# Kernel tuning notes

Hardware: AMD Instinct MI355X
Metric: run time of the kernel (lower is better)

## Reference

```python
import jax, jax.numpy as jnp
import numpy as np

H = 2048
I = 8192
E = 8
EI = I // E  # expert_intermediate_size = 1024


def setup_inputs() -> dict:
    key = jax.random.key(0)
    k1, k2, k3 = jax.random.split(key, 3)
    B, N = 4, 4096
    x = jax.random.normal(k1, (B, N, H), dtype=jnp.float32)
    position_ids = jnp.arange(B * N, dtype=jnp.int64).reshape(B, N)
    gate_up_proj = 0.02 * jax.random.normal(k2, (E, H, EI * 2), dtype=jnp.float32)
    down_proj = 0.02 * jax.random.normal(k3, (E, EI, H), dtype=jnp.float32)
    return {"x": x, "position_ids": position_ids,
            "gate_up_proj": gate_up_proj, "down_proj": down_proj}


def reference(x, position_ids, gate_up_proj, down_proj):
    # x: [B,N,H]; position_ids: [B,N] (or [N]); expert = pos % E.
    B, N, Hdim = x.shape
    if position_ids.ndim == 1:
        position_ids = jnp.broadcast_to(position_ids[None, :], (B, N))
    eids = (position_ids % E).reshape(B * N)
    flat = x.reshape(B * N, Hdim)

    # Modulo routing is perfectly balanced (N % E == 0 with sequential ids),
    # so group tokens by expert (stable sort) and run dense per-expert GEMMs
    # instead of per-token gathered-weight bmm (same math, no weight blowup).
    T = B * N
    order = jnp.argsort(eids)          # stable in jax -> tokens grouped by expert
    xg = flat[order].reshape(E, T // E, Hdim)            # [E, T/E, H]
    gu = jnp.einsum('ebh,ehk->ebk', xg, gate_up_proj)    # [E, T/E, 2*EI]
    gate, up = gu[..., :EI], gu[..., EI:]
    inter = jax.nn.silu(gate) * up                       # [E, T/E, EI]
    outg = jnp.einsum('ebi,eih->ebh', inter, down_proj)  # [E, T/E, H]
    out = jnp.zeros((T, Hdim), dtype=x.dtype).at[order].set(outg.reshape(T, Hdim))
    return out.reshape(B, N, Hdim)
```

## Files before the change

kernel.cpp:

```cpp
#include <hip/hip_runtime.h>
#include <hip/hip_bf16.h>

typedef unsigned short u16;
typedef __attribute__((ext_vector_type(8))) short short8;
typedef __attribute__((ext_vector_type(8))) unsigned short u16x8;
typedef __attribute__((ext_vector_type(4))) float f32x4;

#define H_DIM 2048
#define EI_DIM 1024
#define NEXP 8

template <int V> struct IC { static constexpr int value = V; };

__device__ __forceinline__ u16 f2bf(float f) {
  __hip_bfloat16 h = __float2bfloat16(f);
  return __builtin_bit_cast(unsigned short, h);
}

__device__ __forceinline__ void load_lds16(const void* g, void* lds) {
  __builtin_amdgcn_global_load_lds(
      (const __attribute__((address_space(1))) unsigned int*)g,
      (__attribute__((address_space(3))) unsigned int*)lds, 16, 0, 0);
}

__global__ void hist_kernel(const int* __restrict__ pid, int* __restrict__ hist) {
  int seg = blockIdx.x, lane = threadIdx.x;
  int eid = pid[seg * 64 + lane] & 7;
#pragma unroll
  for (int e = 0; e < NEXP; ++e) {
    unsigned long long m = __ballot(eid == e);
    if (lane == 0) hist[e * 256 + seg] = __popcll(m);
  }
}

__global__ void scan_kernel(const int* __restrict__ hist, int* __restrict__ base,
                            int* __restrict__ offcnt, int T) {
  __shared__ int lds[256];
  int tid = threadIdx.x;
  int v[8], s = 0;
#pragma unroll
  for (int j = 0; j < 8; ++j) { v[j] = hist[tid * 8 + j]; s += v[j]; }
  lds[tid] = s;
  __syncthreads();
  for (int d = 1; d < 256; d <<= 1) {
    int t = (tid >= d) ? lds[tid - d] : 0;
    __syncthreads();
    lds[tid] += t;
    __syncthreads();
  }
  int run = lds[tid] - s;
#pragma unroll
  for (int j = 0; j < 8; ++j) { base[tid * 8 + j] = run; run += v[j]; }
  __syncthreads();
  if (tid < NEXP) {
    int o = base[tid * 256];
    int nx = (tid < NEXP - 1) ? base[(tid + 1) * 256] : T;
    offcnt[tid] = o;
    offcnt[8 + tid] = nx - o;
  }
}

__global__ void rank_kernel(const int* __restrict__ pid, const int* __restrict__ base,
                            int* __restrict__ order) {
  int seg = blockIdx.x, lane = threadIdx.x;
  int t = seg * 64 + lane;
  int eid = pid[t] & 7;
  unsigned long long below = (1ull << lane) - 1ull;
#pragma unroll
  for (int e = 0; e < NEXP; ++e) {
    unsigned long long m = __ballot(eid == e);
    if (eid == e) {
      int r = __popcll(m & below);
      order[base[e * 256 + seg] + r] = t;
    }
  }
}

__global__ __launch_bounds__(256) void transpose_bf16(const float* __restrict__ in,
                                                      u16* __restrict__ out, int R, int C) {
  __shared__ u16 tile[64][65];
  int nbr = R >> 6, nbc = C >> 6;
  int per_e = nbr * nbc;
  int bx = blockIdx.x;
  int e = bx / per_e, rem = bx % per_e;
  int tr = rem % nbr, tc = rem / nbr;
  const float* ine = in + (size_t)e * R * C;
  u16* oute = out + (size_t)e * R * C;
  int r0 = tr * 64, c0 = tc * 64;
  int tid = threadIdx.x;
  int lrow = tid >> 4, lc4 = (tid & 15) * 4;
#pragma unroll
  for (int p = 0; p < 4; ++p) {
    int rl = p * 16 + lrow;
    float4 v = *(const float4*)&ine[(size_t)(r0 + rl) * C + c0 + lc4];
    tile[rl][lc4 + 0] = f2bf(v.x);
    tile[rl][lc4 + 1] = f2bf(v.y);
    tile[rl][lc4 + 2] = f2bf(v.z);
    tile[rl][lc4 + 3] = f2bf(v.w);
  }
  __syncthreads();
#pragma unroll
  for (int q = 0; q < 16; ++q) {
    int idx = q * 256 + tid;
    int jr = idx >> 6, hc = idx & 63;
    oute[(size_t)(c0 + jr) * R + r0 + hc] = tile[hc][jr];
  }
}

__global__ __launch_bounds__(256) void gather_x(const float* __restrict__ x,
                                                const int* __restrict__ order,
                                                u16* __restrict__ xg) {
  int g = blockIdx.x;
  int t = order[g];
  const float* src = x + (size_t)t * H_DIM;
  u16* dst = xg + (size_t)g * H_DIM;
  int c = threadIdx.x * 8;
  float4 a = *(const float4*)&src[c];
  float4 b = *(const float4*)&src[c + 4];
  u16x8 v;
  v[0] = f2bf(a.x); v[1] = f2bf(a.y); v[2] = f2bf(a.z); v[3] = f2bf(a.w);
  v[4] = f2bf(b.x); v[5] = f2bf(b.y); v[6] = f2bf(b.z); v[7] = f2bf(b.w);
  *(u16x8*)&dst[c] = v;
}

template <int KTOT, int KIND>
__global__ __launch_bounds__(512, 2) void gemm8_kernel(
    const u16* __restrict__ A, const u16* __restrict__ Bmat, void* __restrict__ outp,
    const int* __restrict__ offcnt, const int* __restrict__ order, int T, int MT) {
  constexpr int NK = KTOT / 64;
  constexpr int ASTR = (KIND == 0) ? H_DIM : EI_DIM;
  constexpr int BSTR = ASTR;
  constexpr size_t BEXP = (size_t)2048 * BSTR;
  __shared__ u16 As[2][2][8192];
  __shared__ u16 Bs[2][2][8192];

  int nwg = gridDim.x;
  int bid = blockIdx.x;
  int bx = ((nwg & 7) == 0) ? ((bid & 7) * (nwg >> 3) + (bid >> 3)) : bid;

  int nt = bx & 7;
  int rest = bx >> 3;
  int mt = rest % MT;
  int e = rest / MT;
  int off = offcnt[e], cnt = offcnt[8 + e];
  if (mt * 256 >= cnt) return;

  const u16* Be = Bmat + (size_t)e * BEXP;
  int tid = threadIdx.x, w = tid >> 6, l = tid & 63;
  int wm = w >> 2, wn = w & 3, lr = l & 15, lg = l >> 4;

  const u16* aSrc[2];
  const u16* bSrc[2];
#pragma unroll
  for (int j = 0; j < 2; ++j) {
    int r = j * 128 + (tid >> 2);
    int c = tid & 3;
    int sw = (r >> 1) & 3;
    int grow = min(off + mt * 256 + r, T - 1);
    aSrc[j] = A + (size_t)grow * ASTR + ((c ^ sw) * 8);
    int n;
    if (KIND == 0) {
      int q = r >> 4, rr = r & 15;
      n = ((q & 2) ? EI_DIM : 0) + nt * 128 + ((q >> 2) << 5) + ((q & 1) << 4) + rr;
    } else {
      n = nt * 256 + r;
    }
    bSrc[j] = Be + (size_t)n * BSTR + ((c ^ sw) * 8);
  }

  auto stageA = [&](int kt, int kh, int buf) {
#pragma unroll
    for (int j = 0; j < 2; ++j)
      load_lds16(aSrc[j] + kt * 64 + kh * 32, &As[buf][kh][j * 4096 + w * 512]);
  };
  auto stageB = [&](int kt, int kh, int buf) {
#pragma unroll
    for (int j = 0; j < 2; ++j)
      load_lds16(bSrc[j] + kt * 64 + kh * 32, &Bs[buf][kh][j * 4096 + w * 512]);
  };

  int cidx = (lg ^ ((lr >> 1) & 3)) * 8;
  int aRow0 = wm * 128 + lr;
  int bRow0 = wn * 64 + lr;

  short8 av[4], bv[4];
  auto loadA4 = [&](int buf, int kh, int h) {
#pragma unroll
    for (int mm = 0; mm < 4; ++mm)
      av[mm] = *(const short8*)&As[buf][kh][(aRow0 + (h * 4 + mm) * 16) * 32 + cidx];
  };
  auto loadB4 = [&](int buf, int kh) {
#pragma unroll
    for (int nn = 0; nn < 4; ++nn)
      bv[nn] = *(const short8*)&Bs[buf][kh][(bRow0 + nn * 16) * 32 + cidx];
  };

  f32x4 acc[8][4];
#pragma unroll
  for (int m = 0; m < 8; ++m)
#pragma unroll
    for (int nn = 0; nn < 4; ++nn) acc[m][nn] = {0.f, 0.f, 0.f, 0.f};

  auto MFMA_H = [&](auto HC) {
    constexpr int h = decltype(HC)::value;
    __builtin_amdgcn_s_setprio(1);
#pragma unroll
    for (int mm = 0; mm < 4; ++mm)
#pragma unroll
      for (int nn = 0; nn < 4; ++nn)
        acc[h * 4 + mm][nn] =
            __builtin_amdgcn_mfma_f32_16x16x32_bf16(av[mm], bv[nn], acc[h * 4 + mm][nn], 0, 0, 0);
    __builtin_amdgcn_s_setprio(0);
  };

  stageA(0, 0, 0); stageB(0, 0, 0); stageA(0, 1, 0); stageB(0, 1, 0);
  stageB(1, 0, 1); stageA(1, 0, 1); stageB(1, 1, 1);
  asm volatile("s_waitcnt vmcnt(6)" ::: "memory");
  __builtin_amdgcn_s_barrier();
  __builtin_amdgcn_sched_barrier(0);

  auto TILE = [&](int t, auto BC) {
    constexpr int b = decltype(BC)::value;
    constexpr int bn = b ^ 1;
    loadA4(b, 0, 0);
    loadB4(b, 0);
    stageA(t + 1, 1, bn);
    __builtin_amdgcn_s_barrier();
    MFMA_H(IC<0>{});
    __builtin_amdgcn_s_barrier();
    __builtin_amdgcn_sched_barrier(0);
    loadA4(b, 0, 1);
    stageB(t + 2, 0, b);
    __builtin_amdgcn_s_barrier();
    MFMA_H(IC<1>{});
    __builtin_amdgcn_s_barrier();
    __builtin_amdgcn_sched_barrier(0);
    loadA4(b, 1, 0);
    loadB4(b, 1);
    stageA(t + 2, 0, b);
    __builtin_amdgcn_s_barrier();
    MFMA_H(IC<0>{});
    __builtin_amdgcn_s_barrier();
    __builtin_amdgcn_sched_barrier(0);
    loadA4(b, 1, 1);
    stageB(t + 2, 1, b);
    __builtin_amdgcn_s_barrier();
    MFMA_H(IC<1>{});
    asm volatile("s_waitcnt vmcnt(6)" ::: "memory");
    __builtin_amdgcn_s_barrier();
    __builtin_amdgcn_sched_barrier(0);
  };

#pragma unroll 1
  for (int t = 0; t < NK - 3; t += 2) {
    TILE(t, IC<0>{});
    TILE(t + 1, IC<1>{});
  }

  {
    loadA4(0, 0, 0);
    loadB4(0, 0);
    stageA(NK - 1, 1, 1);
    MFMA_H(IC<0>{});
    loadA4(0, 0, 1);
    MFMA_H(IC<1>{});
    loadA4(0, 1, 0);
    loadB4(0, 1);
    MFMA_H(IC<0>{});
    loadA4(0, 1, 1);
    MFMA_H(IC<1>{});
    asm volatile("s_waitcnt vmcnt(0)" ::: "memory");
    __builtin_amdgcn_s_barrier();
    __builtin_amdgcn_sched_barrier(0);
    loadA4(1, 0, 0);
    loadB4(1, 0);
    MFMA_H(IC<0>{});
    loadA4(1, 0, 1);
    MFMA_H(IC<1>{});
    loadA4(1, 1, 0);
    loadB4(1, 1);
    MFMA_H(IC<0>{});
    loadA4(1, 1, 1);
    MFMA_H(IC<1>{});
  }

  if (KIND == 0) {
    u16* inter = (u16*)outp;
#pragma unroll
    for (int m = 0; m < 8; ++m)
#pragma unroll
      for (int nn = 0; nn < 2; ++nn) {
        f32x4 g = acc[m][nn], u = acc[m][nn + 2];
        int icol = nt * 128 + wn * 32 + nn * 16 + lr;
#pragma unroll
        for (int j = 0; j < 4; ++j) {
          int r = wm * 128 + m * 16 + lg * 4 + j;
          int grow = mt * 256 + r;
          if (grow < cnt) {
            float gv = g[j];
            float val = (gv / (1.f + __expf(-gv))) * u[j];
            inter[(size_t)(off + grow) * EI_DIM + icol] = f2bf(val);
          }
        }
      }
  } else {
    float* out = (float*)outp;
#pragma unroll
    for (int m = 0; m < 8; ++m)
#pragma unroll
      for (int nn = 0; nn < 4; ++nn) {
        int ncol = nt * 256 + wn * 64 + nn * 16 + lr;
#pragma unroll
        for (int j = 0; j < 4; ++j) {
          int r = wm * 128 + m * 16 + lg * 4 + j;
          int grow = mt * 256 + r;
          if (grow < cnt) {
            int tt = order[off + grow];
            out[(size_t)tt * H_DIM + ncol] = acc[m][nn][j];
          }
        }
      }
  }
}

extern "C" void kernel_launch(void* const* d_in, const int* in_sizes, int n_in,
                              void* d_out, int out_size, void* d_ws, size_t ws_size,
                              hipStream_t stream) {
  const float* x = (const float*)d_in[0];
  const int* pid = (const int*)d_in[1];
  const float* gup = (const float*)d_in[2];
  const float* dwn = (const float*)d_in[3];
  float* out = (float*)d_out;

  const int T = in_sizes[1];
  const int MT = (T + 255) / 256;

  char* ws = (char*)d_ws;
  size_t o = 0;
  auto take = [&](size_t b) { size_t r = o; o += (b + 255) & ~(size_t)255; return r; };
  int* offcnt = (int*)(ws + take(16 * 4));
  int* hist = (int*)(ws + take(2048 * 4));
  int* base = (int*)(ws + take(2052 * 4));
  int* order = (int*)(ws + take((size_t)T * 4));
  u16* xg = (u16*)(ws + take((size_t)T * H_DIM * 2));
  u16* wguT = (u16*)(ws + take((size_t)NEXP * 2048 * 2048 * 2));
  u16* wdT = (u16*)(ws + take((size_t)NEXP * 2048 * 1024 * 2));
  u16* inter = (u16*)(ws + take((size_t)T * EI_DIM * 2));

  hist_kernel<<<T / 64, 64, 0, stream>>>(pid, hist);
  scan_kernel<<<1, 256, 0, stream>>>(hist, base, offcnt, T);
  rank_kernel<<<T / 64, 64, 0, stream>>>(pid, base, order);
  transpose_bf16<<<NEXP * 32 * 32, 256, 0, stream>>>(gup, wguT, 2048, 2048);
  transpose_bf16<<<NEXP * 16 * 32, 256, 0, stream>>>(dwn, wdT, 1024, 2048);
  gather_x<<<T, 256, 0, stream>>>(x, order, xg);

  gemm8_kernel<2048, 0><<<NEXP * MT * 8, 512, 0, stream>>>(xg, wguT, inter, offcnt, order, T, MT);
  gemm8_kernel<1024, 1><<<NEXP * MT * 8, 512, 0, stream>>>(inter, wdT, out, offcnt, order, T, MT);
}
```

Measured before the change: 353.1 us.

## Make expert GEMMs persistent over fixed grid and stage down-proj output through LDS

```diff
diff --git a/kernel.cpp b/kernel.cpp
--- a/kernel.cpp
+++ b/kernel.cpp
@@ -126,7 +126,7 @@
 template <int KTOT, int KIND>
 __global__ __launch_bounds__(512, 2) void gemm8_kernel(
     const u16* __restrict__ A, const u16* __restrict__ Bmat, void* __restrict__ outp,
-    const int* __restrict__ offcnt, const int* __restrict__ order, int T, int MT) {
+    const int* __restrict__ offcnt, const int* __restrict__ order, int T) {
   constexpr int NK = KTOT / 64;
   constexpr int ASTR = (KIND == 0) ? H_DIM : EI_DIM;
   constexpr int BSTR = ASTR;
@@ -136,190 +136,205 @@
 
   int nwg = gridDim.x;
   int bid = blockIdx.x;
-  int bx = ((nwg & 7) == 0) ? ((bid & 7) * (nwg >> 3) + (bid >> 3)) : bid;
-
-  int nt = bx & 7;
-  int rest = bx >> 3;
-  int mt = rest % MT;
-  int e = rest / MT;
+  int bx = (bid & 7) * (nwg >> 3) + (bid >> 3);
+  int e = bx >> 6;
+  int s = bx & 63;
   int off = offcnt[e], cnt = offcnt[8 + e];
-  if (mt * 256 >= cnt) return;
-
   const u16* Be = Bmat + (size_t)e * BEXP;
+
   int tid = threadIdx.x, w = tid >> 6, l = tid & 63;
   int wm = w >> 2, wn = w & 3, lr = l & 15, lg = l >> 4;
-
-  const u16* aSrc[2];
-  const u16* bSrc[2];
-#pragma unroll
-  for (int j = 0; j < 2; ++j) {
-    int r = j * 128 + (tid >> 2);
-    int c = tid & 3;
-    int sw = (r >> 1) & 3;
-    int grow = min(off + mt * 256 + r, T - 1);
-    aSrc[j] = A + (size_t)grow * ASTR + ((c ^ sw) * 8);
-    int n;
-    if (KIND == 0) {
-      int q = r >> 4, rr = r & 15;
-      n = ((q & 2) ? EI_DIM : 0) + nt * 128 + ((q >> 2) << 5) + ((q & 1) << 4) + rr;
-    } else {
-      n = nt * 256 + r;
-    }
-    bSrc[j] = Be + (size_t)n * BSTR + ((c ^ sw) * 8);
-  }
-
-  auto stageA = [&](int kt, int kh, int buf) {
-#pragma unroll
-    for (int j = 0; j < 2; ++j)
-      load_lds16(aSrc[j] + kt * 64 + kh * 32, &As[buf][kh][j * 4096 + w * 512]);
-  };
-  auto stageB = [&](int kt, int kh, int buf) {
-#pragma unroll
-    for (int j = 0; j < 2; ++j)
-      load_lds16(bSrc[j] + kt * 64 + kh * 32, &Bs[buf][kh][j * 4096 + w * 512]);
-  };
-
   int cidx = (lg ^ ((lr >> 1) & 3)) * 8;
   int aRow0 = wm * 128 + lr;
   int bRow0 = wn * 64 + lr;
-
-  short8 av[4], bv[4];
-  auto loadA4 = [&](int buf, int kh, int h) {
-#pragma unroll
-    for (int mm = 0; mm < 4; ++mm)
-      av[mm] = *(const short8*)&As[buf][kh][(aRow0 + (h * 4 + mm) * 16) * 32 + cidx];
-  };
-  auto loadB4 = [&](int buf, int kh) {
-#pragma unroll
-    for (int nn = 0; nn < 4; ++nn)
-      bv[nn] = *(const short8*)&Bs[buf][kh][(bRow0 + nn * 16) * 32 + cidx];
-  };
-
-  f32x4 acc[8][4];
-#pragma unroll
-  for (int m = 0; m < 8; ++m)
-#pragma unroll
-    for (int nn = 0; nn < 4; ++nn) acc[m][nn] = {0.f, 0.f, 0.f, 0.f};
-
-  auto MFMA_H = [&](auto HC) {
-    constexpr int h = decltype(HC)::value;
-    __builtin_amdgcn_s_setprio(1);
-#pragma unroll
-    for (int mm = 0; mm < 4; ++mm)
+  int sr[2], sc[2];
+#pragma unroll
+  for (int j = 0; j < 2; ++j) {
+    sr[j] = j * 128 + (tid >> 2);
+    int c = tid & 3;
+    sc[j] = (c ^ ((sr[j] >> 1) & 3)) * 8;
+  }
+
+#pragma unroll 1
+  for (int it = s; it < 512; it += 64) {
+    int mt = it >> 3, nt = it & 7;
+    if (mt * 256 >= cnt) continue;
+
+    const u16* aSrc[2];
+    const u16* bSrc[2];
+#pragma unroll
+    for (int j = 0; j < 2; ++j) {
+      int r = sr[j];
+      int grow = min(off + mt * 256 + r, T - 1);
+      aSrc[j] = A + (size_t)grow * ASTR + sc[j];
+      int n;
+      if (KIND == 0) {
+        int q = r >> 4, rr = r & 15;
+        n = ((q & 2) ? EI_DIM : 0) + nt * 128 + ((q >> 2) << 5) + ((q & 1) << 4) + rr;
+      } else {
+        n = nt * 256 + r;
+      }
+      bSrc[j] = Be + (size_t)n * BSTR + sc[j];
+    }
+
+    auto stageA = [&](int kt, int kh, int buf) {
+#pragma unroll
+      for (int j = 0; j < 2; ++j)
+        load_lds16(aSrc[j] + kt * 64 + kh * 32, &As[buf][kh][j * 4096 + w * 512]);
+    };
+    auto stageB = [&](int kt, int kh, int buf) {
+#pragma unroll
+      for (int j = 0; j < 2; ++j)
+        load_lds16(bSrc[j] + kt * 64 + kh * 32, &Bs[buf][kh][j * 4096 + w * 512]);
+    };
+
+    short8 av[4], bv[4];
+    auto loadA4 = [&](int buf, int kh, int h) {
+#pragma unroll
+      for (int mm = 0; mm < 4; ++mm)
+        av[mm] = *(const short8*)&As[buf][kh][(aRow0 + (h * 4 + mm) * 16) * 32 + cidx];
+    };
+    auto loadB4 = [&](int buf, int kh) {
 #pragma unroll
       for (int nn = 0; nn < 4; ++nn)
-        acc[h * 4 + mm][nn] =
-            __builtin_amdgcn_mfma_f32_16x16x32_bf16(av[mm], bv[nn], acc[h * 4 + mm][nn], 0, 0, 0);
-    __builtin_amdgcn_s_setprio(0);
-  };
-
-  stageA(0, 0, 0); stageB(0, 0, 0); stageA(0, 1, 0); stageB(0, 1, 0);
-  stageB(1, 0, 1); stageA(1, 0, 1); stageB(1, 1, 1);
-  asm volatile("s_waitcnt vmcnt(6)" ::: "memory");
-  __builtin_amdgcn_s_barrier();
-  __builtin_amdgcn_sched_barrier(0);
-
-  auto TILE = [&](int t, auto BC) {
-    constexpr int b = decltype(BC)::value;
-    constexpr int bn = b ^ 1;
-    loadA4(b, 0, 0);
-    loadB4(b, 0);
-    stageA(t + 1, 1, bn);
-    __builtin_amdgcn_s_barrier();
-    MFMA_H(IC<0>{});
-    __builtin_amdgcn_s_barrier();
-    __builtin_amdgcn_sched_barrier(0);
-    loadA4(b, 0, 1);
-    stageB(t + 2, 0, b);
-    __builtin_amdgcn_s_barrier();
-    MFMA_H(IC<1>{});
-    __builtin_amdgcn_s_barrier();
-    __builtin_amdgcn_sched_barrier(0);
-    loadA4(b, 1, 0);
-    loadB4(b, 1);
-    stageA(t + 2, 0, b);
-    __builtin_amdgcn_s_barrier();
-    MFMA_H(IC<0>{});
-    __builtin_amdgcn_s_barrier();
-    __builtin_amdgcn_sched_barrier(0);
-    loadA4(b, 1, 1);
-    stageB(t + 2, 1, b);
-    __builtin_amdgcn_s_barrier();
-    MFMA_H(IC<1>{});
+        bv[nn] = *(const short8*)&Bs[buf][kh][(bRow0 + nn * 16) * 32 + cidx];
+    };
+
+    f32x4 acc[8][4];
+#pragma unroll
+    for (int m = 0; m < 8; ++m)
+#pragma unroll
+      for (int nn = 0; nn < 4; ++nn) acc[m][nn] = {0.f, 0.f, 0.f, 0.f};
+
+    auto MFMA_H = [&](auto HC) {
+      constexpr int h = decltype(HC)::value;
+      __builtin_amdgcn_s_setprio(1);
+#pragma unroll
+      for (int mm = 0; mm < 4; ++mm)
+#pragma unroll
+        for (int nn = 0; nn < 4; ++nn)
+          acc[h * 4 + mm][nn] =
+              __builtin_amdgcn_mfma_f32_16x16x32_bf16(av[mm], bv[nn], acc[h * 4 + mm][nn], 0, 0, 0);
+      __builtin_amdgcn_s_setprio(0);
+    };
+
+    __syncthreads();
+
+    stageA(0, 0, 0); stageB(0, 0, 0); stageA(0, 1, 0); stageB(0, 1, 0);
+    stageB(1, 0, 1); stageA(1, 0, 1); stageB(1, 1, 1);
     asm volatile("s_waitcnt vmcnt(6)" ::: "memory");
     __builtin_amdgcn_s_barrier();
     __builtin_amdgcn_sched_barrier(0);
-  };
+
+    auto TILE = [&](int t, auto BC) {
+      constexpr int b = decltype(BC)::value;
+      constexpr int bn = b ^ 1;
+      loadA4(b, 0, 0);
+      loadB4(b, 0);
+      stageA(t + 1, 1, bn);
+      __builtin_amdgcn_s_barrier();
+      MFMA_H(IC<0>{});
+      __builtin_amdgcn_s_barrier();
+      __builtin_amdgcn_sched_barrier(0);
+      loadA4(b, 0, 1);
+      stageB(t + 2, 0, b);
+      __builtin_amdgcn_s_barrier();
+      MFMA_H(IC<1>{});
+      __builtin_amdgcn_s_barrier();
+      __builtin_amdgcn_sched_barrier(0);
+      loadA4(b, 1, 0);
+      loadB4(b, 1);
+      stageA(t + 2, 0, b);
+      __builtin_amdgcn_s_barrier();
+      MFMA_H(IC<0>{});
+      __builtin_amdgcn_s_barrier();
+      __builtin_amdgcn_sched_barrier(0);
+      loadA4(b, 1, 1);
+      stageB(t + 2, 1, b);
+      __builtin_amdgcn_s_barrier();
+      MFMA_H(IC<1>{});
+      asm volatile("s_waitcnt vmcnt(6)" ::: "memory");
+      __builtin_amdgcn_s_barrier();
+      __builtin_amdgcn_sched_barrier(0);
+    };
 
 #pragma unroll 1
-  for (int t = 0; t < NK - 3; t += 2) {
-    TILE(t, IC<0>{});
-    TILE(t + 1, IC<1>{});
-  }
-
-  {
-    loadA4(0, 0, 0);
-    loadB4(0, 0);
-    stageA(NK - 1, 1, 1);
-    MFMA_H(IC<0>{});
-    loadA4(0, 0, 1);
-    MFMA_H(IC<1>{});
-    loadA4(0, 1, 0);
-    loadB4(0, 1);
-    MFMA_H(IC<0>{});
-    loadA4(0, 1, 1);
-    MFMA_H(IC<1>{});
-    asm volatile("s_waitcnt vmcnt(0)" ::: "memory");
-    __builtin_amdgcn_s_barrier();
-    __builtin_amdgcn_sched_barrier(0);
-    loadA4(1, 0, 0);
-    loadB4(1, 0);
-    MFMA_H(IC<0>{});
-    loadA4(1, 0, 1);
-    MFMA_H(IC<1>{});
-    loadA4(1, 1, 0);
-    loadB4(1, 1);
-    MFMA_H(IC<0>{});
-    loadA4(1, 1, 1);
-    MFMA_H(IC<1>{});
-  }
-
-  if (KIND == 0) {
-    u16* inter = (u16*)outp;
-#pragma unroll
-    for (int m = 0; m < 8; ++m)
-#pragma unroll
-      for (int nn = 0; nn < 2; ++nn) {
-        f32x4 g = acc[m][nn], u = acc[m][nn + 2];
-        int icol = nt * 128 + wn * 32 + nn * 16 + lr;
-#pragma unroll
-        for (int j = 0; j < 4; ++j) {
-          int r = wm * 128 + m * 16 + lg * 4 + j;
-          int grow = mt * 256 + r;
+    for (int t = 0; t < NK - 3; t += 2) {
+      TILE(t, IC<0>{});
+      TILE(t + 1, IC<1>{});
+    }
+
+    {
+      loadA4(0, 0, 0);
+      loadB4(0, 0);
+      stageA(NK - 1, 1, 1);
+      MFMA_H(IC<0>{});
+      loadA4(0, 0, 1);
+      MFMA_H(IC<1>{});
+      loadA4(0, 1, 0);
+      loadB4(0, 1);
+      MFMA_H(IC<0>{});
+      loadA4(0, 1, 1);
+      MFMA_H(IC<1>{});
+      asm volatile("s_waitcnt vmcnt(0)" ::: "memory");
+      __builtin_amdgcn_s_barrier();
+      __builtin_amdgcn_sched_barrier(0);
+      loadA4(1, 0, 0);
+      loadB4(1, 0);
+      MFMA_H(IC<0>{});
+      loadA4(1, 0, 1);
+      MFMA_H(IC<1>{});
+      loadA4(1, 1, 0);
+      loadB4(1, 1);
+      MFMA_H(IC<0>{});
+      loadA4(1, 1, 1);
+      MFMA_H(IC<1>{});
+    }
+
+    if (KIND == 0) {
+      u16* inter = (u16*)outp;
+#pragma unroll
+      for (int m = 0; m < 8; ++m)
+#pragma unroll
+        for (int nn = 0; nn < 2; ++nn) {
+          f32x4 g = acc[m][nn], u = acc[m][nn + 2];
+          int icol = nt * 128 + wn * 32 + nn * 16 + lr;
+#pragma unroll
+          for (int j = 0; j < 4; ++j) {
+            int r = wm * 128 + m * 16 + lg * 4 + j;
+            int grow = mt * 256 + r;
+            if (grow < cnt) {
+              float gv = g[j];
+              float val = (gv / (1.f + __expf(-gv))) * u[j];
+              inter[(size_t)(off + grow) * EI_DIM + icol] = f2bf(val);
+            }
+          }
+        }
+    } else {
+      float* out = (float*)outp;
+      float* lf = (float*)&As[0][0][0];
+#pragma unroll
+      for (int m = 0; m < 8; ++m) {
+        __syncthreads();
+#pragma unroll
+        for (int nn = 0; nn < 4; ++nn)
+#pragma unroll
+          for (int j = 0; j < 4; ++j)
+            lf[(wm * 16 + lg * 4 + j) * 256 + wn * 64 + nn * 16 + lr] = acc[m][nn][j];
+        __syncthreads();
+#pragma unroll
+        for (int k = 0; k < 4; ++k) {
+          int idx = tid + k * 512;
+          int rl = idx >> 6, c4 = idx & 63;
+          int grow = mt * 256 + (rl >> 4) * 128 + m * 16 + (rl & 15);
           if (grow < cnt) {
-            float gv = g[j];
-            float val = (gv / (1.f + __expf(-gv))) * u[j];
-            inter[(size_t)(off + grow) * EI_DIM + icol] = f2bf(val);
+            int tt = order[off + grow];
+            *(float4*)&out[(size_t)tt * H_DIM + nt * 256 + c4 * 4] =
+                *(const float4*)&lf[rl * 256 + c4 * 4];
           }
         }
       }
-  } else {
-    float* out = (float*)outp;
-#pragma unroll
-    for (int m = 0; m < 8; ++m)
-#pragma unroll
-      for (int nn = 0; nn < 4; ++nn) {
-        int ncol = nt * 256 + wn * 64 + nn * 16 + lr;
-#pragma unroll
-        for (int j = 0; j < 4; ++j) {
-          int r = wm * 128 + m * 16 + lg * 4 + j;
-          int grow = mt * 256 + r;
-          if (grow < cnt) {
-            int tt = order[off + grow];
-            out[(size_t)tt * H_DIM + ncol] = acc[m][nn][j];
-          }
-        }
-      }
+    }
   }
 }
 
@@ -333,12 +348,11 @@
   float* out = (float*)d_out;
 
   const int T = in_sizes[1];
-  const int MT = (T + 255) / 256;
 
   char* ws = (char*)d_ws;
   size_t o = 0;
   auto take = [&](size_t b) { size_t r = o; o += (b + 255) & ~(size_t)255; return r; };
-  int* offcnt = (int*)(ws + take(16 * 4));
+  int* offcnt = (int*)(ws + take(32 * 4));
   int* hist = (int*)(ws + take(2048 * 4));
   int* base = (int*)(ws + take(2052 * 4));
   int* order = (int*)(ws + take((size_t)T * 4));
@@ -354,6 +368,6 @@
   transpose_bf16<<<NEXP * 16 * 32, 256, 0, stream>>>(dwn, wdT, 1024, 2048);
   gather_x<<<T, 256, 0, stream>>>(x, order, xg);
 
-  gemm8_kernel<2048, 0><<<NEXP * MT * 8, 512, 0, stream>>>(xg, wguT, inter, offcnt, order, T, MT);
-  gemm8_kernel<1024, 1><<<NEXP * MT * 8, 512, 0, stream>>>(inter, wdT, out, offcnt, order, T, MT);
-}
+  gemm8_kernel<2048, 0><<<512, 512, 0, stream>>>(xg, wguT, inter, offcnt, order, T);
+  gemm8_kernel<1024, 1><<<512, 512, 0, stream>>>(inter, wdT, out, offcnt, order, T);
+}
```

After: 336.9 us. 1.05x faster.
